# Performance work log

Hardware: AMD Instinct MI355X
Metric: run time of the kernel (lower is better)

Reference implementation:

```python
import jax, jax.numpy as jnp
import numpy as np

VOCAB = 32000
HID = 1024
CUTOFFS = [0, 10000, 20000, 32000]
N_CLUSTERS = 2
DIV = 4
PROJ_DIMS = [HID // DIV**i for i in range(N_CLUSTERS + 1)]  # [1024, 256, 64]
# Faithful to source quirk: n_vocabs = cutoffs[i] + cutoffs[i+1]
LOGIT_DIMS = [CUTOFFS[i] + CUTOFFS[i + 1] for i in range(N_CLUSTERS + 1)]  # [10000, 30000, 52000]


def setup_inputs() -> dict:
    key = jax.random.key(0)
    ks = jax.random.split(key, 16)
    N = 2048
    inp = {
        "x": jax.random.normal(ks[0], (N, HID), dtype=jnp.float32),
        "y": jax.random.randint(ks[1], (N,), 0, VOCAB, dtype=jnp.int64),
    }
    s = 0.02
    # projections: Linear(hidden, proj_dims[i], bias=False); stored as [in, out]
    inp["Wp0"] = jax.random.normal(ks[2], (HID, PROJ_DIMS[0]), dtype=jnp.float32) * s
    inp["Wp1"] = jax.random.normal(ks[3], (HID, PROJ_DIMS[1]), dtype=jnp.float32) * s
    inp["Wp2"] = jax.random.normal(ks[4], (HID, PROJ_DIMS[2]), dtype=jnp.float32) * s
    # logits: Linear(proj_dims[i], LOGIT_DIMS[i]) with bias
    inp["Wl0"] = jax.random.normal(ks[5], (PROJ_DIMS[0], LOGIT_DIMS[0]), dtype=jnp.float32) * s
    inp["bl0"] = jnp.zeros((LOGIT_DIMS[0],), dtype=jnp.float32)
    inp["Wl1"] = jax.random.normal(ks[6], (PROJ_DIMS[1], LOGIT_DIMS[1]), dtype=jnp.float32) * s
    inp["bl1"] = jnp.zeros((LOGIT_DIMS[1],), dtype=jnp.float32)
    inp["Wl2"] = jax.random.normal(ks[7], (PROJ_DIMS[2], LOGIT_DIMS[2]), dtype=jnp.float32) * s
    inp["bl2"] = jnp.zeros((LOGIT_DIMS[2],), dtype=jnp.float32)
    # cluster_logit: Linear(hidden, n_clusters)
    inp["Wc"] = jax.random.normal(ks[8], (HID, N_CLUSTERS), dtype=jnp.float32) * s
    inp["bc"] = jnp.zeros((N_CLUSTERS,), dtype=jnp.float32)
    return inp


def reference(x, y, Wp0, Wp1, Wp2, Wl0, bl0, Wl1, bl1, Wl2, bl2, Wc, bc):
    # head: project (dim-preserving here) then head-vocab logits + cluster logits
    head_proj = x @ Wp0                                   # [N, 1024]
    head_logit = jnp.concatenate(
        [head_proj @ Wl0 + bl0, head_proj @ Wc + bc], axis=1
    )                                                     # [N, 10000 + 2]
    head_lp = jax.nn.log_softmax(head_logit, axis=1)

    nll = jnp.zeros(y.shape, dtype=x.dtype)

    # cluster 0: targets in [0, cutoffs[1])
    m0 = (y >= CUTOFFS[0]) & (y < CUTOFFS[1])
    t0 = jnp.clip(y - CUTOFFS[0], 0, head_lp.shape[1] - 1)
    lp0 = jnp.take_along_axis(head_lp, t0[:, None], axis=1)[:, 0]
    nll = jnp.where(m0, -lp0, nll)

    # tail clusters: small projection GEMM + log_softmax + gather, combined via masks
    tails = [(Wp1, Wl1, bl1), (Wp2, Wl2, bl2)]
    for i, (Wp, Wl, bl) in enumerate(tails, start=1):
        l, r = CUTOFFS[i], CUTOFFS[i + 1]
        mask = (y >= l) & (y < r)
        t = jnp.clip(y - l, 0, Wl.shape[1] - 1)
        tail_lp = jax.nn.log_softmax((x @ Wp) @ Wl + bl, axis=1)  # [N, LOGIT_DIMS[i]]
        # faithful to source: head column -i (reversed cluster order quirk)
        lp = head_lp[:, -i] + jnp.take_along_axis(tail_lp, t[:, None], axis=1)[:, 0]
        nll = jnp.where(mask, -lp, nll)

    return nll
```

## Files before the change

### kernel.cpp

```cpp
#include <hip/hip_runtime.h>
#include <math.h>

#define HID 1024
#define NROWS 2048

typedef __attribute__((ext_vector_type(8))) short short8;
typedef __attribute__((ext_vector_type(4))) short short4_t;
typedef __attribute__((ext_vector_type(4))) float f32x4;

__device__ __forceinline__ short f2bf(float f) {
  union { float f; unsigned u; } v; v.f = f;
  unsigned r = v.u + 0x7fffu + ((v.u >> 16) & 1u);
  return (short)(r >> 16);
}
__device__ __forceinline__ float bf2f(short s) {
  union { unsigned u; float f; } v; v.u = ((unsigned)(unsigned short)s) << 16;
  return v.f;
}
__device__ __forceinline__ float wave_sum(float a) {
#pragma unroll
  for (int off = 32; off; off >>= 1) a += __shfl_xor(a, off, 64);
  return a;
}

__device__ __forceinline__ void transpose_tile(const float* __restrict__ W,
                                               short* __restrict__ BT,
                                               int K, int N, int Npad, int tn,
                                               int b, int tid) {
  __shared__ float T[32][33];
  const int n0 = (b % tn) * 32, k0 = (b / tn) * 32;
  const int r = tid >> 3, c = (tid & 7) * 4;
  float v0 = 0.f, v1 = 0.f, v2 = 0.f, v3 = 0.f;
  const float* p = &W[(size_t)(k0 + r) * N];
  if (n0 + c + 3 < N) {
    v0 = p[n0 + c]; v1 = p[n0 + c + 1]; v2 = p[n0 + c + 2]; v3 = p[n0 + c + 3];
  } else {
    if (n0 + c + 0 < N) v0 = p[n0 + c + 0];
    if (n0 + c + 1 < N) v1 = p[n0 + c + 1];
    if (n0 + c + 2 < N) v2 = p[n0 + c + 2];
  }
  T[r][c] = v0; T[r][c + 1] = v1; T[r][c + 2] = v2; T[r][c + 3] = v3;
  __syncthreads();
  const int nl = tid >> 3, kl = (tid & 7) * 4;
  const int n = n0 + nl;
  if (n < Npad) {
    short4_t o;
    o.x = (n < N) ? f2bf(T[kl + 0][nl]) : (short)0;
    o.y = (n < N) ? f2bf(T[kl + 1][nl]) : (short)0;
    o.z = (n < N) ? f2bf(T[kl + 2][nl]) : (short)0;
    o.w = (n < N) ? f2bf(T[kl + 3][nl]) : (short)0;
    *(short4_t*)&BT[(size_t)n * K + k0 + kl] = o;
  }
}

__global__ __launch_bounds__(256) void prep(
    const float* __restrict__ x, const int* __restrict__ y,
    const float* __restrict__ Wp0, const float* __restrict__ Wp1,
    const float* __restrict__ Wp2, const float* __restrict__ Wl0,
    short* __restrict__ xb,
    int* __restrict__ counts, int* __restrict__ slot_of_row,
    int* __restrict__ rows1, int* __restrict__ rows2,
    short* __restrict__ T0, short* __restrict__ T1, short* __restrict__ T2,
    short* __restrict__ T3) {
  const int tid = threadIdx.x;
  int b = blockIdx.x;
  if (b == 0) {
    __shared__ int c1s, c2s;
    if (tid == 0) { c1s = 0; c2s = 0; }
    __syncthreads();
    for (int r = tid; r < NROWS; r += 256) {
      const int yy = y[r];
      if (yy >= 20000) {
        const int s = atomicAdd(&c2s, 1);
        slot_of_row[r] = s; rows2[s] = r;
      } else if (yy >= 10000) {
        const int s = atomicAdd(&c1s, 1);
        slot_of_row[r] = s; rows1[s] = r;
      } else {
        slot_of_row[r] = -1;
      }
    }
    __syncthreads();
    if (tid == 0) { counts[0] = NROWS; counts[1] = c1s; counts[2] = c2s; }
    return;
  }
  if (b <= 2048) {
    const int i = ((b - 1) * 256 + tid) * 4;
    short4_t o;
    o.x = f2bf(x[i + 0]); o.y = f2bf(x[i + 1]);
    o.z = f2bf(x[i + 2]); o.w = f2bf(x[i + 3]);
    *(short4_t*)&xb[i] = o;
    return;
  }
  b -= 2049;
  if (b < 1024)               transpose_tile(Wp0, T0, 1024, 1024, 1024, 32, b, tid);
  else if ((b -= 1024) < 256) transpose_tile(Wp1, T1, 1024, 256, 256, 8, b, tid);
  else if ((b -= 256) < 128)  transpose_tile(Wp2, T2, 1024, 64, 128, 4, b, tid);
  else { b -= 128;            transpose_tile(Wl0, T3, 1024, 10000, 10112, 316, b, tid); }
}

__device__ __forceinline__ void mfma_mainloop(const short* aB[4], const short* bB[4],
                                              short* As, short* Bs,
                                              f32x4 acc[4][4],
                                              int K, int w, int lane) {
  const int quad = lane >> 4, ln = lane & 15;
  const int wm = w >> 1, wn = w & 1;
  const int l7 = ln & 7;
  for (int kt = 0; kt < K; kt += 64) {
#pragma unroll
    for (int i = 0; i < 4; ++i) {
      const int row = w * 32 + i * 8;
      __builtin_amdgcn_global_load_lds(
          (const __attribute__((address_space(1))) void*)(aB[i] + kt),
          (__attribute__((address_space(3))) void*)(As + row * 64), 16, 0, 0);
      __builtin_amdgcn_global_load_lds(
          (const __attribute__((address_space(1))) void*)(bB[i] + kt),
          (__attribute__((address_space(3))) void*)(Bs + row * 64), 16, 0, 0);
    }
    __syncthreads();
#pragma unroll
    for (int ks = 0; ks < 2; ++ks) {
      const int kcs = ks * 4 + quad;
      short8 af[4], bfr[4];
#pragma unroll
      for (int mt = 0; mt < 4; ++mt) {
        const int row = wm * 64 + mt * 16 + ln;
        af[mt] = *(const short8*)(As + ((row * 8 + (kcs ^ l7)) << 3));
      }
#pragma unroll
      for (int nt = 0; nt < 4; ++nt) {
        const int rowb = wn * 64 + nt * 16 + ln;
        bfr[nt] = *(const short8*)(Bs + ((rowb * 8 + (kcs ^ l7)) << 3));
      }
#pragma unroll
      for (int mt = 0; mt < 4; ++mt)
#pragma unroll
        for (int nt = 0; nt < 4; ++nt)
          acc[mt][nt] = __builtin_amdgcn_mfma_f32_16x16x32_bf16(
              af[mt], bfr[nt], acc[mt][nt], 0, 0, 0);
    }
    __syncthreads();
  }
}


__global__ __launch_bounds__(256) void proj_all(
    const short* __restrict__ xb,
    const short* __restrict__ WpT0, const short* __restrict__ WpT1,
    const short* __restrict__ WpT2,
    short* __restrict__ P0b, short* __restrict__ P1c, short* __restrict__ P2c,
    const int* __restrict__ rows1, const int* __restrict__ rows2,
    const int* __restrict__ counts) {
  int b = blockIdx.x;
  const int tid = threadIdx.x;
  const short* BT; short* C; int N, r0, c0, cnt;
  const int* rowlist = nullptr;
  if (b < 128) {
    BT = WpT0; C = P0b; N = 1024;
    c0 = (b & 7) * 128; r0 = (b >> 3) * 128; cnt = NROWS;
  } else if (b < 160) {
    b -= 128; BT = WpT1; C = P1c; N = 256;
    c0 = (b & 1) * 128; r0 = (b >> 1) * 128; rowlist = rows1; cnt = counts[1];
  } else {
    b -= 160; BT = WpT2; C = P2c; N = 64;
    c0 = 0; r0 = b * 128; rowlist = rows2; cnt = counts[2];
  }
  if (r0 >= cnt) return;

  __shared__ short As[128 * 64];
  __shared__ short Bs[128 * 64];
  const int w = tid >> 6, lane = tid & 63;
  const int quad = lane >> 4, ln = lane & 15;
  const int wm = w >> 1, wn = w & 1;
  const int rsub = lane >> 3;
  const int kc = (lane & 7) ^ rsub;
  const int K = 1024;

  const short* aB[4]; const short* bB[4];
#pragma unroll
  for (int i = 0; i < 4; ++i) {
    const int sl = r0 + w * 32 + i * 8 + rsub;
    const int ar = rowlist ? rowlist[sl < cnt ? sl : cnt - 1] : sl;
    aB[i] = xb + (size_t)ar * K + kc * 8;
    bB[i] = BT + (size_t)(c0 + w * 32 + i * 8 + rsub) * K + kc * 8;
  }

  f32x4 acc[4][4];
  const f32x4 zero = {0.f, 0.f, 0.f, 0.f};
#pragma unroll
  for (int i = 0; i < 4; ++i)
#pragma unroll
    for (int j = 0; j < 4; ++j) acc[i][j] = zero;
  mfma_mainloop(aB, bB, As, Bs, acc, K, w, lane);
#pragma unroll
  for (int mt = 0; mt < 4; ++mt)
#pragma unroll
    for (int r = 0; r < 4; ++r) {
      const int grow = r0 + wm * 64 + mt * 16 + quad * 4 + r;
#pragma unroll
      for (int nt = 0; nt < 4; ++nt) {
        const int cg = c0 + wn * 64 + nt * 16 + ln;
        if (cg < N) C[(size_t)grow * N + cg] = f2bf(acc[mt][nt][r]);
      }
    }
}

template <int K, int NCOLS, int NSPLIT, bool CS_SLOW>
__device__ __forceinline__ void logit_phase(
    const short* __restrict__ A, const short* __restrict__ BT,
    const float* __restrict__ bias, float* __restrict__ ps,
    short* As, short* Bs,
    int nrb, int csbase, int ncs, int lid, int step, int tid) {
  float* psL = (float*)As;
  const int w = tid >> 6, lane = tid & 63;
  const int quad = lane >> 4, ln = lane & 15;
  const int wm = w >> 1, wn = w & 1;
  const int rsub = lane >> 3;
  const int kc = (lane & 7) ^ rsub;
  const int l7 = ln & 7;
  const int T = nrb * ncs;
  for (int t = lid; t < T; t += step) {
    const int rb = CS_SLOW ? (t % nrb) : (t / ncs);
    const int cs = csbase + (CS_SLOW ? (t / nrb) : (t % ncs));
    const int r0 = rb * 128, c0 = cs * 128;

    const short* aB[4]; const short* bB[4];
#pragma unroll
    for (int i = 0; i < 4; ++i) {
      aB[i] = A + (size_t)(r0 + w * 32 + i * 8 + rsub) * K + kc * 8;
      bB[i] = BT + (size_t)(c0 + w * 32 + i * 8 + rsub) * K + kc * 8;
    }
    f32x4 acc[4][4];
    const f32x4 zero = {0.f, 0.f, 0.f, 0.f};
#pragma unroll
    for (int i = 0; i < 4; ++i)
#pragma unroll
      for (int j = 0; j < 4; ++j) acc[i][j] = zero;

    __syncthreads();
    for (int kt = 0; kt < K; kt += 64) {
#pragma unroll
      for (int i = 0; i < 4; ++i) {
        const int row = w * 32 + i * 8;
        __builtin_amdgcn_global_load_lds(
            (const __attribute__((address_space(1))) void*)(aB[i] + kt),
            (__attribute__((address_space(3))) void*)(As + row * 64), 16, 0, 0);
        __builtin_amdgcn_global_load_lds(
            (const __attribute__((address_space(1))) void*)(bB[i] + kt),
            (__attribute__((address_space(3))) void*)(Bs + row * 64), 16, 0, 0);
      }
      __syncthreads();
#pragma unroll
      for (int ks = 0; ks < 2; ++ks) {
        const int kcs = ks * 4 + quad;
        short8 af[4], bfr[4];
#pragma unroll
        for (int mt = 0; mt < 4; ++mt) {
          const int row = wm * 64 + mt * 16 + ln;
          af[mt] = *(const short8*)(As + ((row * 8 + (kcs ^ l7)) << 3));
        }
#pragma unroll
        for (int nt = 0; nt < 4; ++nt) {
          const int rowb = wn * 64 + nt * 16 + ln;
          bfr[nt] = *(const short8*)(Bs + ((rowb * 8 + (kcs ^ l7)) << 3));
        }
#pragma unroll
        for (int mt = 0; mt < 4; ++mt)
#pragma unroll
          for (int nt = 0; nt < 4; ++nt)
            acc[mt][nt] = __builtin_amdgcn_mfma_f32_16x16x32_bf16(
                af[mt], bfr[nt], acc[mt][nt], 0, 0, 0);
      }
      __syncthreads();
    }

    float bv[4];
#pragma unroll
    for (int nt = 0; nt < 4; ++nt) {
      const int cg = c0 + wn * 64 + nt * 16 + ln;
      bv[nt] = (cg < NCOLS) ? bias[cg] : -1.0e30f;
    }
#pragma unroll
    for (int mt = 0; mt < 4; ++mt)
#pragma unroll
      for (int r = 0; r < 4; ++r) {
        float s = 0.f;
#pragma unroll
        for (int nt = 0; nt < 4; ++nt)
          s += __expf(acc[mt][nt][r] + bv[nt]);
#pragma unroll
        for (int off = 1; off < 16; off <<= 1) s += __shfl_xor(s, off, 64);
        if (ln == 0) psL[wn * 128 + wm * 64 + mt * 16 + quad * 4 + r] = s;
      }
    __syncthreads();
    if (tid < 128)
      ps[(size_t)(r0 + tid) * NSPLIT + cs] = psL[tid] + psL[128 + tid];
  }
}

__global__ __launch_bounds__(256) void head_mix(
    const short* __restrict__ P0b, const short* __restrict__ WlT0,
    const float* __restrict__ bl0, float* __restrict__ psh,
    const float* __restrict__ Wl1, const float* __restrict__ Wl2,
    short* __restrict__ WlT1, short* __restrict__ WlT2) {
  int b = blockIdx.x;
  const int tid = threadIdx.x;
  if (b >= 1280) {
    b -= 1280;
    if (b < 7520) transpose_tile(Wl1, WlT1, 256, 30000, 30080, 940, b, tid);
    else          transpose_tile(Wl2, WlT2, 64, 52000, 52096, 1628, b - 7520, tid);
    return;
  }
  __shared__ short As[128 * 64];
  __shared__ short Bs[128 * 64];
  const int xcd = b & 7;
  const int j = b >> 3;
  const int nch = (xcd < 7) ? 10 : 9;
  logit_phase<1024, 10000, 79, false>(P0b, WlT0, bl0, psh, As, Bs,
                                      16, xcd * 10, nch, j, 100000, tid);
}

__global__ __launch_bounds__(256) void tail_logit(
    const short* __restrict__ P1c, const short* __restrict__ WlT1,
    const float* __restrict__ bl1, float* __restrict__ ps1,
    const short* __restrict__ P2c, const short* __restrict__ WlT2,
    const float* __restrict__ bl2, float* __restrict__ ps2,
    const int* __restrict__ counts) {
  __shared__ short As[128 * 64];
  __shared__ short Bs[128 * 64];
  const int tid = threadIdx.x;
  const int xcd = blockIdx.x & 7;
  const int lid = blockIdx.x >> 3;
  const int nrb1 = (counts[1] + 127) >> 7;
  const int nrb2 = (counts[2] + 127) >> 7;
  logit_phase<256, 30000, 235, true>(P1c, WlT1, bl1, ps1, As, Bs,
                                     nrb1, xcd * 30, (xcd < 7) ? 30 : 25,
                                     lid, 128, tid);
  logit_phase<64, 52000, 407, true>(P2c, WlT2, bl2, ps2, As, Bs,
                                    nrb2, xcd * 51, (xcd < 7) ? 51 : 50,
                                    lid, 128, tid);
}

__global__ __launch_bounds__(256) void finalize(
    const short* __restrict__ P0b, const short* __restrict__ P1c,
    const short* __restrict__ P2c,
    const short* __restrict__ WlT0, const float* __restrict__ bl0,
    const short* __restrict__ WlT1, const float* __restrict__ bl1,
    const short* __restrict__ WlT2, const float* __restrict__ bl2,
    const float* __restrict__ Wc, const float* __restrict__ bc,
    const int* __restrict__ y, const int* __restrict__ slot_of_row,
    const float* __restrict__ psh, const float* __restrict__ ps1,
    const float* __restrict__ ps2, float* __restrict__ out) {
  const int lane = threadIdx.x & 63;
  const int row = blockIdx.x * 4 + (threadIdx.x >> 6);

  float a0 = 0.f, a1 = 0.f;
  for (int k = lane; k < HID; k += 64) {
    const float p = bf2f(P0b[(size_t)row * HID + k]);
    a0 += p * Wc[2 * k];
    a1 += p * Wc[2 * k + 1];
  }
  a0 = wave_sum(a0);
  a1 = wave_sum(a1);
  const float cl0 = a0 + bc[0], cl1 = a1 + bc[1];

  float S = 0.f;
  for (int i = lane; i < 79; i += 64) S += psh[(size_t)row * 79 + i];
  S = wave_sum(S) + __expf(cl0) + __expf(cl1);
  const float lse = logf(S);

  const int yy = y[row];
  float nll;
  if (yy < 10000) {
    const short* pr = P0b + (size_t)row * 1024;
    const short* wr = WlT0 + (size_t)yy * 1024;
    float a = 0.f;
    for (int kk = lane * 4; kk < 1024; kk += 256) {
      const short4_t p = *(const short4_t*)(pr + kk);
      const short4_t wv = *(const short4_t*)(wr + kk);
      a += bf2f(p.x) * bf2f(wv.x) + bf2f(p.y) * bf2f(wv.y)
         + bf2f(p.z) * bf2f(wv.z) + bf2f(p.w) * bf2f(wv.w);
    }
    a = wave_sum(a);
    nll = -((a + bl0[yy]) - lse);
  } else if (yy < 20000) {
    const int t = yy - 10000;
    const int slot = slot_of_row[row];
    float S1 = 0.f;
    for (int i = lane; i < 235; i += 64) S1 += ps1[(size_t)slot * 235 + i];
    S1 = wave_sum(S1);
    const short* pr = P1c + (size_t)slot * 256;
    const short* wr = WlT1 + (size_t)t * 256;
    const int kk = lane * 4;
    const short4_t p = *(const short4_t*)(pr + kk);
    const short4_t wv = *(const short4_t*)(wr + kk);
    float a = bf2f(p.x) * bf2f(wv.x) + bf2f(p.y) * bf2f(wv.y)
            + bf2f(p.z) * bf2f(wv.z) + bf2f(p.w) * bf2f(wv.w);
    a = wave_sum(a);
    nll = -((cl1 - lse) + ((a + bl1[t]) - logf(S1)));
  } else {
    const int t = yy - 20000;
    const int slot = slot_of_row[row];
    float S2 = 0.f;
    for (int i = lane; i < 407; i += 64) S2 += ps2[(size_t)slot * 407 + i];
    S2 = wave_sum(S2);
    float a = 0.f;
    if (lane < 16) {
      const short* pr = P2c + (size_t)slot * 64;
      const short* wr = WlT2 + (size_t)t * 64;
      const int kk = lane * 4;
      const short4_t p = *(const short4_t*)(pr + kk);
      const short4_t wv = *(const short4_t*)(wr + kk);
      a = bf2f(p.x) * bf2f(wv.x) + bf2f(p.y) * bf2f(wv.y)
        + bf2f(p.z) * bf2f(wv.z) + bf2f(p.w) * bf2f(wv.w);
    }
    a = wave_sum(a);
    nll = -((cl0 - lse) + ((a + bl2[t]) - logf(S2)));
  }
  if (lane == 0) out[row] = nll;
}

extern "C" void kernel_launch(void* const* d_in, const int* in_sizes, int n_in,
                              void* d_out, int out_size, void* d_ws, size_t ws_size,
                              hipStream_t stream) {
  const float* x   = (const float*)d_in[0];
  const int*   y   = (const int*)d_in[1];
  const float* Wp0 = (const float*)d_in[2];
  const float* Wp1 = (const float*)d_in[3];
  const float* Wp2 = (const float*)d_in[4];
  const float* Wl0 = (const float*)d_in[5];
  const float* bl0 = (const float*)d_in[6];
  const float* Wl1 = (const float*)d_in[7];
  const float* bl1 = (const float*)d_in[8];
  const float* Wl2 = (const float*)d_in[9];
  const float* bl2 = (const float*)d_in[10];
  const float* Wc  = (const float*)d_in[11];
  const float* bc  = (const float*)d_in[12];
  float* out = (float*)d_out;

  float* fws = (float*)d_ws;
  float* psh = fws; fws += (size_t)NROWS * 79;
  float* ps1 = fws; fws += (size_t)NROWS * 235;
  float* ps2 = fws; fws += (size_t)NROWS * 407;
  int* iws = (int*)fws;
  int* counts      = iws; iws += 4;
  int* slot_of_row = iws; iws += NROWS;
  int* rows1       = iws; iws += NROWS;
  int* rows2       = iws; iws += NROWS;
  short* sp = (short*)iws;
  short* xb   = sp; sp += (size_t)NROWS * 1024;
  short* P0b  = sp; sp += (size_t)NROWS * 1024;
  short* P1c  = sp; sp += (size_t)NROWS * 256;
  short* P2c  = sp; sp += (size_t)NROWS * 64;
  short* WpT0 = sp; sp += (size_t)1024 * 1024;
  short* WpT1 = sp; sp += (size_t)256 * 1024;
  short* WpT2 = sp; sp += (size_t)128 * 1024;
  short* WlT0 = sp; sp += (size_t)10112 * 1024;
  short* WlT1 = sp; sp += (size_t)30080 * 256;
  short* WlT2 = sp; sp += (size_t)52096 * 64;

  dim3 blk(256);
  prep<<<dim3(13569), blk, 0, stream>>>(x, y, Wp0, Wp1, Wp2, Wl0, xb,
                                        counts, slot_of_row, rows1, rows2,
                                        WpT0, WpT1, WpT2, WlT0);
  proj_all<<<dim3(176), blk, 0, stream>>>(xb, WpT0, WpT1, WpT2,
                                          P0b, P1c, P2c, rows1, rows2, counts);
  head_mix<<<dim3(12056), blk, 0, stream>>>(P0b, WlT0, bl0, psh,
                                            Wl1, Wl2, WlT1, WlT2);
  tail_logit<<<dim3(1024), blk, 0, stream>>>(P1c, WlT1, bl1, ps1,
                                             P2c, WlT2, bl2, ps2, counts);
  finalize<<<dim3(NROWS / 4), blk, 0, stream>>>(
      P0b, P1c, P2c, WlT0, bl0, WlT1, bl1, WlT2, bl2, Wc, bc, y, slot_of_row,
      psh, ps1, ps2, out);
}
```

Baseline: 322.8 us.

## Merge all stages into one cooperative persistent kernel with grid syncs

```diff
diff --git a/kernel.cpp b/kernel.cpp
--- a/kernel.cpp
+++ b/kernel.cpp
@@ -1,5 +1,8 @@
 #include <hip/hip_runtime.h>
+#include <hip/hip_cooperative_groups.h>
 #include <math.h>
+
+namespace cg = cooperative_groups;
 
 #define HID 1024
 #define NROWS 2048
@@ -23,11 +26,21 @@
   return a;
 }
 
+struct Params {
+  const float* x; const int* y;
+  const float *Wp0, *Wp1, *Wp2, *Wl0, *bl0, *Wl1, *bl1, *Wl2, *bl2, *Wc, *bc;
+  short* xb;
+  int *counts, *slot_of_row, *rows1, *rows2;
+  short *WpT0, *WpT1, *WpT2, *WlT0, *WlT1, *WlT2;
+  short *P0b, *P1c, *P2c;
+  float *psh, *ps1, *ps2, *out;
+};
+
 __device__ __forceinline__ void transpose_tile(const float* __restrict__ W,
                                                short* __restrict__ BT,
                                                int K, int N, int Npad, int tn,
-                                               int b, int tid) {
-  __shared__ float T[32][33];
+                                               int b, int tid, float* T) {
+  __syncthreads();
   const int n0 = (b % tn) * 32, k0 = (b / tn) * 32;
   const int r = tid >> 3, c = (tid & 7) * 4;
   float v0 = 0.f, v1 = 0.f, v2 = 0.f, v3 = 0.f;
@@ -39,170 +52,59 @@
     if (n0 + c + 1 < N) v1 = p[n0 + c + 1];
     if (n0 + c + 2 < N) v2 = p[n0 + c + 2];
   }
-  T[r][c] = v0; T[r][c + 1] = v1; T[r][c + 2] = v2; T[r][c + 3] = v3;
+  T[r * 33 + c] = v0; T[r * 33 + c + 1] = v1;
+  T[r * 33 + c + 2] = v2; T[r * 33 + c + 3] = v3;
   __syncthreads();
   const int nl = tid >> 3, kl = (tid & 7) * 4;
   const int n = n0 + nl;
   if (n < Npad) {
     short4_t o;
-    o.x = (n < N) ? f2bf(T[kl + 0][nl]) : (short)0;
-    o.y = (n < N) ? f2bf(T[kl + 1][nl]) : (short)0;
-    o.z = (n < N) ? f2bf(T[kl + 2][nl]) : (short)0;
-    o.w = (n < N) ? f2bf(T[kl + 3][nl]) : (short)0;
+    o.x = (n < N) ? f2bf(T[(kl + 0) * 33 + nl]) : (short)0;
+    o.y = (n < N) ? f2bf(T[(kl + 1) * 33 + nl]) : (short)0;
+    o.z = (n < N) ? f2bf(T[(kl + 2) * 33 + nl]) : (short)0;
+    o.w = (n < N) ? f2bf(T[(kl + 3) * 33 + nl]) : (short)0;
     *(short4_t*)&BT[(size_t)n * K + k0 + kl] = o;
   }
 }
 
-__global__ __launch_bounds__(256) void prep(
-    const float* __restrict__ x, const int* __restrict__ y,
-    const float* __restrict__ Wp0, const float* __restrict__ Wp1,
-    const float* __restrict__ Wp2, const float* __restrict__ Wl0,
-    short* __restrict__ xb,
-    int* __restrict__ counts, int* __restrict__ slot_of_row,
-    int* __restrict__ rows1, int* __restrict__ rows2,
-    short* __restrict__ T0, short* __restrict__ T1, short* __restrict__ T2,
-    short* __restrict__ T3) {
-  const int tid = threadIdx.x;
-  int b = blockIdx.x;
-  if (b == 0) {
-    __shared__ int c1s, c2s;
-    if (tid == 0) { c1s = 0; c2s = 0; }
+__device__ __forceinline__ void prep_unit(const Params& p, int u, int tid,
+                                          float* T, int* cnt_s) {
+  if (u == 0) {
+    if (tid == 0) { cnt_s[0] = 0; cnt_s[1] = 0; }
     __syncthreads();
     for (int r = tid; r < NROWS; r += 256) {
-      const int yy = y[r];
+      const int yy = p.y[r];
       if (yy >= 20000) {
-        const int s = atomicAdd(&c2s, 1);
-        slot_of_row[r] = s; rows2[s] = r;
+        const int s = atomicAdd(&cnt_s[1], 1);
+        p.slot_of_row[r] = s; p.rows2[s] = r;
       } else if (yy >= 10000) {
-        const int s = atomicAdd(&c1s, 1);
-        slot_of_row[r] = s; rows1[s] = r;
+        const int s = atomicAdd(&cnt_s[0], 1);
+        p.slot_of_row[r] = s; p.rows1[s] = r;
       } else {
-        slot_of_row[r] = -1;
-      }
-    }
-    __syncthreads();
-    if (tid == 0) { counts[0] = NROWS; counts[1] = c1s; counts[2] = c2s; }
+        p.slot_of_row[r] = -1;
+      }
+    }
+    __syncthreads();
+    if (tid == 0) {
+      p.counts[0] = NROWS; p.counts[1] = cnt_s[0]; p.counts[2] = cnt_s[1];
+    }
     return;
   }
-  if (b <= 2048) {
-    const int i = ((b - 1) * 256 + tid) * 4;
+  if (u <= 2048) {
+    const int i = ((u - 1) * 256 + tid) * 4;
     short4_t o;
-    o.x = f2bf(x[i + 0]); o.y = f2bf(x[i + 1]);
-    o.z = f2bf(x[i + 2]); o.w = f2bf(x[i + 3]);
-    *(short4_t*)&xb[i] = o;
+    o.x = f2bf(p.x[i + 0]); o.y = f2bf(p.x[i + 1]);
+    o.z = f2bf(p.x[i + 2]); o.w = f2bf(p.x[i + 3]);
+    *(short4_t*)&p.xb[i] = o;
     return;
   }
-  b -= 2049;
-  if (b < 1024)               transpose_tile(Wp0, T0, 1024, 1024, 1024, 32, b, tid);
-  else if ((b -= 1024) < 256) transpose_tile(Wp1, T1, 1024, 256, 256, 8, b, tid);
-  else if ((b -= 256) < 128)  transpose_tile(Wp2, T2, 1024, 64, 128, 4, b, tid);
-  else { b -= 128;            transpose_tile(Wl0, T3, 1024, 10000, 10112, 316, b, tid); }
-}
-
-__device__ __forceinline__ void mfma_mainloop(const short* aB[4], const short* bB[4],
-                                              short* As, short* Bs,
-                                              f32x4 acc[4][4],
-                                              int K, int w, int lane) {
-  const int quad = lane >> 4, ln = lane & 15;
-  const int wm = w >> 1, wn = w & 1;
-  const int l7 = ln & 7;
-  for (int kt = 0; kt < K; kt += 64) {
-#pragma unroll
-    for (int i = 0; i < 4; ++i) {
-      const int row = w * 32 + i * 8;
-      __builtin_amdgcn_global_load_lds(
-          (const __attribute__((address_space(1))) void*)(aB[i] + kt),
-          (__attribute__((address_space(3))) void*)(As + row * 64), 16, 0, 0);
-      __builtin_amdgcn_global_load_lds(
-          (const __attribute__((address_space(1))) void*)(bB[i] + kt),
-          (__attribute__((address_space(3))) void*)(Bs + row * 64), 16, 0, 0);
-    }
-    __syncthreads();
-#pragma unroll
-    for (int ks = 0; ks < 2; ++ks) {
-      const int kcs = ks * 4 + quad;
-      short8 af[4], bfr[4];
-#pragma unroll
-      for (int mt = 0; mt < 4; ++mt) {
-        const int row = wm * 64 + mt * 16 + ln;
-        af[mt] = *(const short8*)(As + ((row * 8 + (kcs ^ l7)) << 3));
-      }
-#pragma unroll
-      for (int nt = 0; nt < 4; ++nt) {
-        const int rowb = wn * 64 + nt * 16 + ln;
-        bfr[nt] = *(const short8*)(Bs + ((rowb * 8 + (kcs ^ l7)) << 3));
-      }
-#pragma unroll
-      for (int mt = 0; mt < 4; ++mt)
-#pragma unroll
-        for (int nt = 0; nt < 4; ++nt)
-          acc[mt][nt] = __builtin_amdgcn_mfma_f32_16x16x32_bf16(
-              af[mt], bfr[nt], acc[mt][nt], 0, 0, 0);
-    }
-    __syncthreads();
-  }
-}
-
-
-__global__ __launch_bounds__(256) void proj_all(
-    const short* __restrict__ xb,
-    const short* __restrict__ WpT0, const short* __restrict__ WpT1,
-    const short* __restrict__ WpT2,
-    short* __restrict__ P0b, short* __restrict__ P1c, short* __restrict__ P2c,
-    const int* __restrict__ rows1, const int* __restrict__ rows2,
-    const int* __restrict__ counts) {
-  int b = blockIdx.x;
-  const int tid = threadIdx.x;
-  const short* BT; short* C; int N, r0, c0, cnt;
-  const int* rowlist = nullptr;
-  if (b < 128) {
-    BT = WpT0; C = P0b; N = 1024;
-    c0 = (b & 7) * 128; r0 = (b >> 3) * 128; cnt = NROWS;
-  } else if (b < 160) {
-    b -= 128; BT = WpT1; C = P1c; N = 256;
-    c0 = (b & 1) * 128; r0 = (b >> 1) * 128; rowlist = rows1; cnt = counts[1];
-  } else {
-    b -= 160; BT = WpT2; C = P2c; N = 64;
-    c0 = 0; r0 = b * 128; rowlist = rows2; cnt = counts[2];
-  }
-  if (r0 >= cnt) return;
-
-  __shared__ short As[128 * 64];
-  __shared__ short Bs[128 * 64];
-  const int w = tid >> 6, lane = tid & 63;
-  const int quad = lane >> 4, ln = lane & 15;
-  const int wm = w >> 1, wn = w & 1;
-  const int rsub = lane >> 3;
-  const int kc = (lane & 7) ^ rsub;
-  const int K = 1024;
-
-  const short* aB[4]; const short* bB[4];
-#pragma unroll
-  for (int i = 0; i < 4; ++i) {
-    const int sl = r0 + w * 32 + i * 8 + rsub;
-    const int ar = rowlist ? rowlist[sl < cnt ? sl : cnt - 1] : sl;
-    aB[i] = xb + (size_t)ar * K + kc * 8;
-    bB[i] = BT + (size_t)(c0 + w * 32 + i * 8 + rsub) * K + kc * 8;
-  }
-
-  f32x4 acc[4][4];
-  const f32x4 zero = {0.f, 0.f, 0.f, 0.f};
-#pragma unroll
-  for (int i = 0; i < 4; ++i)
-#pragma unroll
-    for (int j = 0; j < 4; ++j) acc[i][j] = zero;
-  mfma_mainloop(aB, bB, As, Bs, acc, K, w, lane);
-#pragma unroll
-  for (int mt = 0; mt < 4; ++mt)
-#pragma unroll
-    for (int r = 0; r < 4; ++r) {
-      const int grow = r0 + wm * 64 + mt * 16 + quad * 4 + r;
-#pragma unroll
-      for (int nt = 0; nt < 4; ++nt) {
-        const int cg = c0 + wn * 64 + nt * 16 + ln;
-        if (cg < N) C[(size_t)grow * N + cg] = f2bf(acc[mt][nt][r]);
-      }
-    }
+  int t = u - 2049;
+  if (t < 1024)                transpose_tile(p.Wp0, p.WpT0, 1024, 1024, 1024, 32, t, tid, T);
+  else if ((t -= 1024) < 256)  transpose_tile(p.Wp1, p.WpT1, 1024, 256, 256, 8, t, tid, T);
+  else if ((t -= 256) < 128)   transpose_tile(p.Wp2, p.WpT2, 1024, 64, 128, 4, t, tid, T);
+  else if ((t -= 128) < 10112) transpose_tile(p.Wl0, p.WlT0, 1024, 10000, 10112, 316, t, tid, T);
+  else if ((t -= 10112) < 7520) transpose_tile(p.Wl1, p.WlT1, 256, 30000, 30080, 940, t, tid, T);
+  else { t -= 7520;            transpose_tile(p.Wl2, p.WlT2, 64, 52000, 52096, 1628, t, tid, T); }
 }
 
 template <int K, int NCOLS, int NSPLIT, bool CS_SLOW>
@@ -298,178 +200,279 @@
   }
 }
 
-__global__ __launch_bounds__(256) void head_mix(
-    const short* __restrict__ P0b, const short* __restrict__ WlT0,
-    const float* __restrict__ bl0, float* __restrict__ psh,
-    const float* __restrict__ Wl1, const float* __restrict__ Wl2,
-    short* __restrict__ WlT1, short* __restrict__ WlT2) {
-  int b = blockIdx.x;
-  const int tid = threadIdx.x;
-  if (b >= 1280) {
-    b -= 1280;
-    if (b < 7520) transpose_tile(Wl1, WlT1, 256, 30000, 30080, 940, b, tid);
-    else          transpose_tile(Wl2, WlT2, 64, 52000, 52096, 1628, b - 7520, tid);
-    return;
-  }
-  __shared__ short As[128 * 64];
-  __shared__ short Bs[128 * 64];
-  const int xcd = b & 7;
-  const int j = b >> 3;
-  const int nch = (xcd < 7) ? 10 : 9;
-  logit_phase<1024, 10000, 79, false>(P0b, WlT0, bl0, psh, As, Bs,
-                                      16, xcd * 10, nch, j, 100000, tid);
-}
-
-__global__ __launch_bounds__(256) void tail_logit(
-    const short* __restrict__ P1c, const short* __restrict__ WlT1,
-    const float* __restrict__ bl1, float* __restrict__ ps1,
-    const short* __restrict__ P2c, const short* __restrict__ WlT2,
-    const float* __restrict__ bl2, float* __restrict__ ps2,
-    const int* __restrict__ counts) {
+__device__ __forceinline__ void logit_block(const Params& p, int bid, int tid,
+                                            int step, short* As, short* Bs) {
+  const int xcd = bid & 7;
+  const int lid = bid >> 3;
+  const int nrb1 = (p.counts[1] + 127) >> 7;
+  const int nrb2 = (p.counts[2] + 127) >> 7;
+  logit_phase<1024, 10000, 79, false>(p.P0b, p.WlT0, p.bl0, p.psh, As, Bs,
+                                      16, xcd * 10, (xcd < 7) ? 10 : 9,
+                                      lid, step, tid);
+  logit_phase<256, 30000, 235, true>(p.P1c, p.WlT1, p.bl1, p.ps1, As, Bs,
+                                     nrb1, xcd * 30, (xcd < 7) ? 30 : 25,
+                                     lid, step, tid);
+  logit_phase<64, 52000, 407, true>(p.P2c, p.WlT2, p.bl2, p.ps2, As, Bs,
+                                    nrb2, xcd * 51, (xcd < 7) ? 51 : 50,
+                                    lid, step, tid);
+}
+
+__device__ __forceinline__ void proj_tile(const Params& p, int b, int tid,
+                                          short* As, short* Bs) {
+  const short* BT; short* C; int N, r0, c0, cnt;
+  const int* rowlist = nullptr;
+  if (b < 128) {
+    BT = p.WpT0; C = p.P0b; N = 1024;
+    c0 = (b & 7) * 128; r0 = (b >> 3) * 128; cnt = NROWS;
+  } else if (b < 160) {
+    b -= 128; BT = p.WpT1; C = p.P1c; N = 256;
+    c0 = (b & 1) * 128; r0 = (b >> 1) * 128; rowlist = p.rows1; cnt = p.counts[1];
+  } else {
+    b -= 160; BT = p.WpT2; C = p.P2c; N = 64;
+    c0 = 0; r0 = b * 128; rowlist = p.rows2; cnt = p.counts[2];
+  }
+  if (r0 >= cnt) return;
+
+  const int w = tid >> 6, lane = tid & 63;
+  const int quad = lane >> 4, ln = lane & 15;
+  const int wm = w >> 1, wn = w & 1;
+  const int rsub = lane >> 3;
+  const int kc = (lane & 7) ^ rsub;
+  const int l7 = ln & 7;
+  const int K = 1024;
+
+  const short* aB[4]; const short* bB[4];
+#pragma unroll
+  for (int i = 0; i < 4; ++i) {
+    const int sl = r0 + w * 32 + i * 8 + rsub;
+    const int ar = rowlist ? rowlist[sl < cnt ? sl : cnt - 1] : sl;
+    aB[i] = p.xb + (size_t)ar * K + kc * 8;
+    bB[i] = BT + (size_t)(c0 + w * 32 + i * 8 + rsub) * K + kc * 8;
+  }
+
+  f32x4 acc[4][4];
+  const f32x4 zero = {0.f, 0.f, 0.f, 0.f};
+#pragma unroll
+  for (int i = 0; i < 4; ++i)
+#pragma unroll
+    for (int j = 0; j < 4; ++j) acc[i][j] = zero;
+  __syncthreads();
+  for (int kt = 0; kt < K; kt += 64) {
+#pragma unroll
+    for (int i = 0; i < 4; ++i) {
+      const int row = w * 32 + i * 8;
+      __builtin_amdgcn_global_load_lds(
+          (const __attribute__((address_space(1))) void*)(aB[i] + kt),
+          (__attribute__((address_space(3))) void*)(As + row * 64), 16, 0, 0);
+      __builtin_amdgcn_global_load_lds(
+          (const __attribute__((address_space(1))) void*)(bB[i] + kt),
+          (__attribute__((address_space(3))) void*)(Bs + row * 64), 16, 0, 0);
+    }
+    __syncthreads();
+#pragma unroll
+    for (int ks = 0; ks < 2; ++ks) {
+      const int kcs = ks * 4 + quad;
+      short8 af[4], bfr[4];
+#pragma unroll
+      for (int mt = 0; mt < 4; ++mt) {
+        const int row = wm * 64 + mt * 16 + ln;
+        af[mt] = *(const short8*)(As + ((row * 8 + (kcs ^ l7)) << 3));
+      }
+#pragma unroll
+      for (int nt = 0; nt < 4; ++nt) {
+        const int rowb = wn * 64 + nt * 16 + ln;
+        bfr[nt] = *(const short8*)(Bs + ((rowb * 8 + (kcs ^ l7)) << 3));
+      }
+#pragma unroll
+      for (int mt = 0; mt < 4; ++mt)
+#pragma unroll
+        for (int nt = 0; nt < 4; ++nt)
+          acc[mt][nt] = __builtin_amdgcn_mfma_f32_16x16x32_bf16(
+              af[mt], bfr[nt], acc[mt][nt], 0, 0, 0);
+    }
+    __syncthreads();
+  }
+#pragma unroll
+  for (int mt = 0; mt < 4; ++mt)
+#pragma unroll
+    for (int r = 0; r < 4; ++r) {
+      const int grow = r0 + wm * 64 + mt * 16 + quad * 4 + r;
+#pragma unroll
+      for (int nt = 0; nt < 4; ++nt) {
+        const int cg = c0 + wn * 64 + nt * 16 + ln;
+        if (cg < N) C[(size_t)grow * N + cg] = f2bf(acc[mt][nt][r]);
+      }
+    }
+}
+
+__device__ __forceinline__ void finalize_rows(const Params& p, int u, int tid) {
+  const int lane = tid & 63;
+  const int row = u * 4 + (tid >> 6);
+
+  float a0 = 0.f, a1 = 0.f;
+  for (int k = lane; k < HID; k += 64) {
+    const float pv = bf2f(p.P0b[(size_t)row * HID + k]);
+    a0 += pv * p.Wc[2 * k];
+    a1 += pv * p.Wc[2 * k + 1];
+  }
+  a0 = wave_sum(a0);
+  a1 = wave_sum(a1);
+  const float cl0 = a0 + p.bc[0], cl1 = a1 + p.bc[1];
+
+  float S = 0.f;
+  for (int i = lane; i < 79; i += 64) S += p.psh[(size_t)row * 79 + i];
+  S = wave_sum(S) + __expf(cl0) + __expf(cl1);
+  const float lse = logf(S);
+
+  const int yy = p.y[row];
+  float nll;
+  if (yy < 10000) {
+    const short* pr = p.P0b + (size_t)row * 1024;
+    const short* wr = p.WlT0 + (size_t)yy * 1024;
+    float a = 0.f;
+    for (int kk = lane * 4; kk < 1024; kk += 256) {
+      const short4_t pv = *(const short4_t*)(pr + kk);
+      const short4_t wv = *(const short4_t*)(wr + kk);
+      a += bf2f(pv.x) * bf2f(wv.x) + bf2f(pv.y) * bf2f(wv.y)
+         + bf2f(pv.z) * bf2f(wv.z) + bf2f(pv.w) * bf2f(wv.w);
+    }
+    a = wave_sum(a);
+    nll = -((a + p.bl0[yy]) - lse);
+  } else if (yy < 20000) {
+    const int t = yy - 10000;
+    const int slot = p.slot_of_row[row];
+    float S1 = 0.f;
+    for (int i = lane; i < 235; i += 64) S1 += p.ps1[(size_t)slot * 235 + i];
+    S1 = wave_sum(S1);
+    const short* pr = p.P1c + (size_t)slot * 256;
+    const short* wr = p.WlT1 + (size_t)t * 256;
+    const int kk = lane * 4;
+    const short4_t pv = *(const short4_t*)(pr + kk);
+    const short4_t wv = *(const short4_t*)(wr + kk);
+    float a = bf2f(pv.x) * bf2f(wv.x) + bf2f(pv.y) * bf2f(wv.y)
+            + bf2f(pv.z) * bf2f(wv.z) + bf2f(pv.w) * bf2f(wv.w);
+    a = wave_sum(a);
+    nll = -((cl1 - lse) + ((a + p.bl1[t]) - logf(S1)));
+  } else {
+    const int t = yy - 20000;
+    const int slot = p.slot_of_row[row];
+    float S2 = 0.f;
+    for (int i = lane; i < 407; i += 64) S2 += p.ps2[(size_t)slot * 407 + i];
+    S2 = wave_sum(S2);
+    float a = 0.f;
+    if (lane < 16) {
+      const short* pr = p.P2c + (size_t)slot * 64;
+      const short* wr = p.WlT2 + (size_t)t * 64;
+      const int kk = lane * 4;
+      const short4_t pv = *(const short4_t*)(pr + kk);
+      const short4_t wv = *(const short4_t*)(wr + kk);
+      a = bf2f(pv.x) * bf2f(wv.x) + bf2f(pv.y) * bf2f(wv.y)
+        + bf2f(pv.z) * bf2f(wv.z) + bf2f(pv.w) * bf2f(wv.w);
+    }
+    a = wave_sum(a);
+    nll = -((cl0 - lse) + ((a + p.bl2[t]) - logf(S2)));
+  }
+  if (lane == 0) p.out[row] = nll;
+}
+
+__global__ __launch_bounds__(256) void mega(Params p, int nb) {
+  cg::grid_group grid = cg::this_grid();
   __shared__ short As[128 * 64];
   __shared__ short Bs[128 * 64];
   const int tid = threadIdx.x;
-  const int xcd = blockIdx.x & 7;
-  const int lid = blockIdx.x >> 3;
-  const int nrb1 = (counts[1] + 127) >> 7;
-  const int nrb2 = (counts[2] + 127) >> 7;
-  logit_phase<256, 30000, 235, true>(P1c, WlT1, bl1, ps1, As, Bs,
-                                     nrb1, xcd * 30, (xcd < 7) ? 30 : 25,
-                                     lid, 128, tid);
-  logit_phase<64, 52000, 407, true>(P2c, WlT2, bl2, ps2, As, Bs,
-                                    nrb2, xcd * 51, (xcd < 7) ? 51 : 50,
-                                    lid, 128, tid);
-}
-
-__global__ __launch_bounds__(256) void finalize(
-    const short* __restrict__ P0b, const short* __restrict__ P1c,
-    const short* __restrict__ P2c,
-    const short* __restrict__ WlT0, const float* __restrict__ bl0,
-    const short* __restrict__ WlT1, const float* __restrict__ bl1,
-    const short* __restrict__ WlT2, const float* __restrict__ bl2,
-    const float* __restrict__ Wc, const float* __restrict__ bc,
-    const int* __restrict__ y, const int* __restrict__ slot_of_row,
-    const float* __restrict__ psh, const float* __restrict__ ps1,
-    const float* __restrict__ ps2, float* __restrict__ out) {
-  const int lane = threadIdx.x & 63;
-  const int row = blockIdx.x * 4 + (threadIdx.x >> 6);
-
-  float a0 = 0.f, a1 = 0.f;
-  for (int k = lane; k < HID; k += 64) {
-    const float p = bf2f(P0b[(size_t)row * HID + k]);
-    a0 += p * Wc[2 * k];
-    a1 += p * Wc[2 * k + 1];
-  }
-  a0 = wave_sum(a0);
-  a1 = wave_sum(a1);
-  const float cl0 = a0 + bc[0], cl1 = a1 + bc[1];
-
-  float S = 0.f;
-  for (int i = lane; i < 79; i += 64) S += psh[(size_t)row * 79 + i];
-  S = wave_sum(S) + __expf(cl0) + __expf(cl1);
-  const float lse = logf(S);
-
-  const int yy = y[row];
-  float nll;
-  if (yy < 10000) {
-    const short* pr = P0b + (size_t)row * 1024;
-    const short* wr = WlT0 + (size_t)yy * 1024;
-    float a = 0.f;
-    for (int kk = lane * 4; kk < 1024; kk += 256) {
-      const short4_t p = *(const short4_t*)(pr + kk);
-      const short4_t wv = *(const short4_t*)(wr + kk);
-      a += bf2f(p.x) * bf2f(wv.x) + bf2f(p.y) * bf2f(wv.y)
-         + bf2f(p.z) * bf2f(wv.z) + bf2f(p.w) * bf2f(wv.w);
-    }
-    a = wave_sum(a);
-    nll = -((a + bl0[yy]) - lse);
-  } else if (yy < 20000) {
-    const int t = yy - 10000;
-    const int slot = slot_of_row[row];
-    float S1 = 0.f;
-    for (int i = lane; i < 235; i += 64) S1 += ps1[(size_t)slot * 235 + i];
-    S1 = wave_sum(S1);
-    const short* pr = P1c + (size_t)slot * 256;
-    const short* wr = WlT1 + (size_t)t * 256;
-    const int kk = lane * 4;
-    const short4_t p = *(const short4_t*)(pr + kk);
-    const short4_t wv = *(const short4_t*)(wr + kk);
-    float a = bf2f(p.x) * bf2f(wv.x) + bf2f(p.y) * bf2f(wv.y)
-            + bf2f(p.z) * bf2f(wv.z) + bf2f(p.w) * bf2f(wv.w);
-    a = wave_sum(a);
-    nll = -((cl1 - lse) + ((a + bl1[t]) - logf(S1)));
-  } else {
-    const int t = yy - 20000;
-    const int slot = slot_of_row[row];
-    float S2 = 0.f;
-    for (int i = lane; i < 407; i += 64) S2 += ps2[(size_t)slot * 407 + i];
-    S2 = wave_sum(S2);
-    float a = 0.f;
-    if (lane < 16) {
-      const short* pr = P2c + (size_t)slot * 64;
-      const short* wr = WlT2 + (size_t)t * 64;
-      const int kk = lane * 4;
-      const short4_t p = *(const short4_t*)(pr + kk);
-      const short4_t wv = *(const short4_t*)(wr + kk);
-      a = bf2f(p.x) * bf2f(wv.x) + bf2f(p.y) * bf2f(wv.y)
-        + bf2f(p.z) * bf2f(wv.z) + bf2f(p.w) * bf2f(wv.w);
-    }
-    a = wave_sum(a);
-    nll = -((cl0 - lse) + ((a + bl2[t]) - logf(S2)));
-  }
-  if (lane == 0) out[row] = nll;
+  const int bid = blockIdx.x;
+  float* T = (float*)As;
+  int* cnt_s = (int*)Bs;
+
+  for (int u = bid; u < 24345; u += nb) prep_unit(p, u, tid, T, cnt_s);
+  __threadfence();
+  grid.sync();
+
+  if (bid < 176) proj_tile(p, bid, tid, As, Bs);
+  __threadfence();
+  grid.sync();
+
+  logit_block(p, bid, tid, nb >> 3, As, Bs);
+  __threadfence();
+  grid.sync();
+
+  for (int u = bid; u < 512; u += nb) finalize_rows(p, u, tid);
+}
+
+__global__ __launch_bounds__(256) void fb_prep(Params p) {
+  __shared__ float T[32 * 33];
+  __shared__ int cnt_s[2];
+  prep_unit(p, blockIdx.x, threadIdx.x, T, cnt_s);
+}
+__global__ __launch_bounds__(256) void fb_proj(Params p) {
+  __shared__ short As[128 * 64];
+  __shared__ short Bs[128 * 64];
+  proj_tile(p, blockIdx.x, threadIdx.x, As, Bs);
+}
+__global__ __launch_bounds__(256) void fb_logit(Params p) {
+  __shared__ short As[128 * 64];
+  __shared__ short Bs[128 * 64];
+  logit_block(p, blockIdx.x, threadIdx.x, 128, As, Bs);
+}
+__global__ __launch_bounds__(256) void fb_final(Params p) {
+  finalize_rows(p, blockIdx.x, threadIdx.x);
 }
 
 extern "C" void kernel_launch(void* const* d_in, const int* in_sizes, int n_in,
                               void* d_out, int out_size, void* d_ws, size_t ws_size,
                               hipStream_t stream) {
-  const float* x   = (const float*)d_in[0];
-  const int*   y   = (const int*)d_in[1];
-  const float* Wp0 = (const float*)d_in[2];
-  const float* Wp1 = (const float*)d_in[3];
-  const float* Wp2 = (const float*)d_in[4];
-  const float* Wl0 = (const float*)d_in[5];
-  const float* bl0 = (const float*)d_in[6];
-  const float* Wl1 = (const float*)d_in[7];
-  const float* bl1 = (const float*)d_in[8];
-  const float* Wl2 = (const float*)d_in[9];
-  const float* bl2 = (const float*)d_in[10];
-  const float* Wc  = (const float*)d_in[11];
-  const float* bc  = (const float*)d_in[12];
-  float* out = (float*)d_out;
+  Params p;
+  p.x   = (const float*)d_in[0];
+  p.y   = (const int*)d_in[1];
+  p.Wp0 = (const float*)d_in[2];
+  p.Wp1 = (const float*)d_in[3];
+  p.Wp2 = (const float*)d_in[4];
+  p.Wl0 = (const float*)d_in[5];
+  p.bl0 = (const float*)d_in[6];
+  p.Wl1 = (const float*)d_in[7];
+  p.bl1 = (const float*)d_in[8];
+  p.Wl2 = (const float*)d_in[9];
+  p.bl2 = (const float*)d_in[10];
+  p.Wc  = (const float*)d_in[11];
+  p.bc  = (const float*)d_in[12];
+  p.out = (float*)d_out;
 
   float* fws = (float*)d_ws;
-  float* psh = fws; fws += (size_t)NROWS * 79;
-  float* ps1 = fws; fws += (size_t)NROWS * 235;
-  float* ps2 = fws; fws += (size_t)NROWS * 407;
+  p.psh = fws; fws += (size_t)NROWS * 79;
+  p.ps1 = fws; fws += (size_t)NROWS * 235;
+  p.ps2 = fws; fws += (size_t)NROWS * 407;
   int* iws = (int*)fws;
-  int* counts      = iws; iws += 4;
-  int* slot_of_row = iws; iws += NROWS;
-  int* rows1       = iws; iws += NROWS;
-  int* rows2       = iws; iws += NROWS;
+  p.counts      = iws; iws += 4;
+  p.slot_of_row = iws; iws += NROWS;
+  p.rows1       = iws; iws += NROWS;
+  p.rows2       = iws; iws += NROWS;
   short* sp = (short*)iws;
-  short* xb   = sp; sp += (size_t)NROWS * 1024;
-  short* P0b  = sp; sp += (size_t)NROWS * 1024;
-  short* P1c  = sp; sp += (size_t)NROWS * 256;
-  short* P2c  = sp; sp += (size_t)NROWS * 64;
-  short* WpT0 = sp; sp += (size_t)1024 * 1024;
-  short* WpT1 = sp; sp += (size_t)256 * 1024;
-  short* WpT2 = sp; sp += (size_t)128 * 1024;
-  short* WlT0 = sp; sp += (size_t)10112 * 1024;
-  short* WlT1 = sp; sp += (size_t)30080 * 256;
-  short* WlT2 = sp; sp += (size_t)52096 * 64;
-
-  dim3 blk(256);
-  prep<<<dim3(13569), blk, 0, stream>>>(x, y, Wp0, Wp1, Wp2, Wl0, xb,
-                                        counts, slot_of_row, rows1, rows2,
-                                        WpT0, WpT1, WpT2, WlT0);
-  proj_all<<<dim3(176), blk, 0, stream>>>(xb, WpT0, WpT1, WpT2,
-                                          P0b, P1c, P2c, rows1, rows2, counts);
-  head_mix<<<dim3(12056), blk, 0, stream>>>(P0b, WlT0, bl0, psh,
-                                            Wl1, Wl2, WlT1, WlT2);
-  tail_logit<<<dim3(1024), blk, 0, stream>>>(P1c, WlT1, bl1, ps1,
-                                             P2c, WlT2, bl2, ps2, counts);
-  finalize<<<dim3(NROWS / 4), blk, 0, stream>>>(
-      P0b, P1c, P2c, WlT0, bl0, WlT1, bl1, WlT2, bl2, Wc, bc, y, slot_of_row,
-      psh, ps1, ps2, out);
-}
+  p.xb   = sp; sp += (size_t)NROWS * 1024;
+  p.P0b  = sp; sp += (size_t)NROWS * 1024;
+  p.P1c  = sp; sp += (size_t)NROWS * 256;
+  p.P2c  = sp; sp += (size_t)NROWS * 64;
+  p.WpT0 = sp; sp += (size_t)1024 * 1024;
+  p.WpT1 = sp; sp += (size_t)256 * 1024;
+  p.WpT2 = sp; sp += (size_t)128 * 1024;
+  p.WlT0 = sp; sp += (size_t)10112 * 1024;
+  p.WlT1 = sp; sp += (size_t)30080 * 256;
+  p.WlT2 = sp; sp += (size_t)52096 * 64;
+
+  int occ = 0;
+  hipError_t qe = hipOccupancyMaxActiveBlocksPerMultiprocessor(&occ, mega, 256, 0);
+  int nb = (qe == hipSuccess) ? occ * 256 : 0;
+  if (nb > 1024) nb = 1024;
+  nb &= ~7;
+
+  if (nb >= 256) {
+    void* args[] = {(void*)&p, (void*)&nb};
+    hipLaunchCooperativeKernel((const void*)mega, dim3(nb), dim3(256),
+                               args, 0, stream);
+  } else {
+    dim3 blk(256);
+    fb_prep<<<dim3(24345), blk, 0, stream>>>(p);
+    fb_proj<<<dim3(176), blk, 0, stream>>>(p);
+    fb_logit<<<dim3(1024), blk, 0, stream>>>(p);
+    fb_final<<<dim3(512), blk, 0, stream>>>(p);
+  }
+}
```

Measured after the change: 652.8 us. +102.3%, slower.
